# Kernel optimization log

Measured on AMD Instinct MI355X. Metric: run time of the kernel, lower is better.

## Reference

```python
import jax, jax.numpy as jnp
import numpy as np

N_SRC = 100000   # source nodes (columns of adj)
N_DST = 50000    # target nodes (rows of adj)
N_EDGES = 3200000
N_IN = 256
N_OUT = 128


def setup_inputs() -> dict:
    key = jax.random.key(0)
    k = jax.random.split(key, 7)
    stdv = 1.0 / np.sqrt(N_IN)
    x = jax.random.normal(k[0], (N_SRC, N_IN), dtype=jnp.float32)
    W = jax.random.uniform(k[1], (N_OUT, N_IN), minval=-stdv, maxval=stdv, dtype=jnp.float32)
    b = jax.random.uniform(k[2], (N_OUT,), minval=-stdv, maxval=stdv, dtype=jnp.float32)
    adj_rows = jax.random.randint(k[3], (N_EDGES,), 0, N_DST)
    adj_cols = jax.random.randint(k[4], (N_EDGES,), 0, N_SRC)
    # mean-aggregation-style normalized weights (generic positive values)
    adj_vals = jax.random.uniform(k[5], (N_EDGES,), dtype=jnp.float32)
    previous_index = jax.random.randint(k[6], (N_DST,), 0, N_SRC)
    return {"x": x, "W": W, "b": b, "adj_vals": adj_vals,
            "adj_rows": adj_rows, "adj_cols": adj_cols,
            "previous_index": previous_index}


def reference(x, W, b, adj_vals, adj_rows, adj_cols, previous_index):
    # linear projection: h = x @ W.T + b            -> [N_SRC, n_out]
    h = jnp.einsum('ni,oi->no', x, W) + b
    # spmm(adj, h) via COO gather + segment-sum      -> [N_DST, n_out]
    msgs = adj_vals[:, None] * h[adj_cols]          # [E, n_out]
    support = jax.ops.segment_sum(msgs, adj_rows, num_segments=previous_index.shape[0])
    # gather self features and concat                -> [N_DST, 2*n_out]
    return jnp.concatenate([h[previous_index], support], axis=1)
```

## Files before the change

### kernel.cpp

```cpp
#include <hip/hip_runtime.h>
#include <hip/hip_bf16.h>

#define N_IN      256
#define N_OUTC    128
#define RPS       64
#define RPS_SHIFT 6
#define NSB_MAX   1024
#define TILE      4096
#define EPT       16
#define SPILL_CAP 8192

typedef __attribute__((ext_vector_type(8))) short bf16x8;
typedef __attribute__((ext_vector_type(4))) float f32x4;
typedef unsigned short ushort_t;
typedef unsigned int uint_t;

__device__ inline unsigned short f2bf(float f) {
    unsigned u = __float_as_uint(f);
    unsigned r = u + 0x7fffu + ((u >> 16) & 1u);
    return (unsigned short)(r >> 16);
}
__device__ inline float bf_lo(uint_t g) { return __uint_as_float(g << 16); }
__device__ inline float bf_hi(uint_t g) { return __uint_as_float(g & 0xFFFF0000u); }

__global__ void cvtW_kernel(const float* __restrict__ W, ushort_t* __restrict__ wb, int n) {
    int i = blockIdx.x * blockDim.x + threadIdx.x;
    if (i < n) wb[i] = f2bf(W[i]);
}

__global__ __launch_bounds__(256) void fused_build_gemm_kernel(
        const int* __restrict__ rows, const int* __restrict__ cols,
        const float* __restrict__ vals, int E,
        int* __restrict__ sbCount, int2* __restrict__ sbList, int sbCap, int nsb,
        int* __restrict__ spillCnt, int4* __restrict__ spill, int nbBuild,
        const float* __restrict__ x, const ushort_t* __restrict__ wb,
        const float* __restrict__ b, ushort_t* __restrict__ h16) {
    __shared__ int cur[NSB_MAX];
    __shared__ int gbase[NSB_MAX];
    const int tid = threadIdx.x;

    if (blockIdx.x < (uint_t)nbBuild) {
        const int base = blockIdx.x * TILE;
        for (int i = tid; i < nsb; i += 256) cur[i] = 0;
        __syncthreads();

        int comb[EPT];
        #pragma unroll
        for (int k = 0; k < EPT; k++) {
            int e = base + tid + k * 256;
            comb[k] = -1;
            if (e < E) {
                int sb = rows[e] >> RPS_SHIFT;
                int rk = atomicAdd(&cur[sb], 1);
                comb[k] = (sb << 13) | rk;
            }
        }
        __syncthreads();

        for (int i = tid; i < nsb; i += 256)
            gbase[i] = cur[i] ? atomicAdd(&sbCount[i], cur[i]) : 0;
        __syncthreads();

        #pragma unroll
        for (int k = 0; k < EPT; k++) {
            if (comb[k] < 0) continue;
            int e  = base + tid + k * 256;
            int sb = ((uint_t)comb[k]) >> 13;
            int rk = comb[k] & 0x1FFF;
            int r = rows[e], c = cols[e];
            int ev = __float_as_int(vals[e]);
            int pos = gbase[sb] + rk;
            if (pos < sbCap) {
                sbList[(size_t)sb * sbCap + pos] = make_int2(c | ((r & (RPS - 1)) << 17), ev);
            } else {
                int sp = atomicAdd(spillCnt, 1);
                if (sp < SPILL_CAP)
                    spill[sp] = make_int4(r, c, ev, 0);
            }
        }
        return;
    }

    const int blk  = blockIdx.x - nbBuild;
    const int wave = tid >> 6;
    const int lane = tid & 63;
    const int quad = lane >> 4;
    const int l16  = lane & 15;
    const int m0   = blk * 16;
    const int colbase = wave * 32;

    f32x4 acc0 = {0.f, 0.f, 0.f, 0.f};
    f32x4 acc1 = {0.f, 0.f, 0.f, 0.f};

    const float* xrow = x + (size_t)(m0 + l16) * N_IN + quad * 8;
    const ushort_t* w0 = wb + (size_t)(colbase + l16) * N_IN + quad * 8;
    const ushort_t* w1 = w0 + 16 * N_IN;

    #pragma unroll
    for (int kb = 0; kb < N_IN; kb += 32) {
        float4 a0 = *(const float4*)(xrow + kb);
        float4 a1 = *(const float4*)(xrow + kb + 4);
        union { bf16x8 v; __hip_bfloat162 h2[4]; } u;
        u.h2[0] = __float22bfloat162_rn(make_float2(a0.x, a0.y));
        u.h2[1] = __float22bfloat162_rn(make_float2(a0.z, a0.w));
        u.h2[2] = __float22bfloat162_rn(make_float2(a1.x, a1.y));
        u.h2[3] = __float22bfloat162_rn(make_float2(a1.z, a1.w));
        bf16x8 bf0 = *(const bf16x8*)(w0 + kb);
        bf16x8 bf1 = *(const bf16x8*)(w1 + kb);
        acc0 = __builtin_amdgcn_mfma_f32_16x16x32_bf16(u.v, bf0, acc0, 0, 0, 0);
        acc1 = __builtin_amdgcn_mfma_f32_16x16x32_bf16(u.v, bf1, acc1, 0, 0, 0);
    }

    const int c0 = colbase + l16;
    const int c1 = c0 + 16;
    const float bv0 = b[c0];
    const float bv1 = b[c1];
    ushort_t* hp = h16 + (size_t)(m0 + quad * 4) * N_OUTC;
    #pragma unroll
    for (int r = 0; r < 4; r++) {
        hp[(size_t)r * N_OUTC + c0] = f2bf(acc0[r] + bv0);
        hp[(size_t)r * N_OUTC + c1] = f2bf(acc1[r] + bv1);
    }
}

__global__ __launch_bounds__(1024) void sbscan_kernel(const int* __restrict__ sbCount, int sbCap,
                                                      int* __restrict__ sbBase, int nsb) {
    __shared__ int a[NSB_MAX], bsh[NSB_MAX];
    int tid = threadIdx.x;
    int v = 0;
    if (tid < nsb) { v = sbCount[tid]; if (v > sbCap) v = sbCap; }
    a[tid] = v; __syncthreads();
    int* src = a; int* dst = bsh;
    for (int off = 1; off < 1024; off <<= 1) {
        dst[tid] = src[tid] + ((tid >= off) ? src[tid - off] : 0);
        __syncthreads();
        int* t = src; src = dst; dst = t;
    }
    if (tid < nsb) sbBase[tid] = tid ? src[tid - 1] : 0;
}

__global__ __launch_bounds__(256) void sort_kernel(const int* __restrict__ sbCount,
                                                   const int* __restrict__ sbBase,
                                                   const int2* __restrict__ sbList, int sbCap,
                                                   int2* __restrict__ csr,
                                                   int* __restrict__ rowStart, int* __restrict__ rowCnt,
                                                   int Ndst) {
    __shared__ int hist[RPS];
    __shared__ int scanA[RPS];
    __shared__ int curx[RPS];
    const int sb  = blockIdx.x;
    const int tid = threadIdx.x;
    int len = sbCount[sb]; if (len > sbCap) len = sbCap;
    const int base = sbBase[sb];
    const int2* lp = sbList + (size_t)sb * sbCap;

    if (tid < RPS) hist[tid] = 0;
    __syncthreads();

    int i = tid;
    for (; i + 768 < len; i += 1024) {
        int x0 = lp[i].x, x1 = lp[i + 256].x, x2 = lp[i + 512].x, x3 = lp[i + 768].x;
        atomicAdd(&hist[((uint_t)x0) >> 17], 1);
        atomicAdd(&hist[((uint_t)x1) >> 17], 1);
        atomicAdd(&hist[((uint_t)x2) >> 17], 1);
        atomicAdd(&hist[((uint_t)x3) >> 17], 1);
    }
    for (; i < len; i += 256) atomicAdd(&hist[((uint_t)lp[i].x) >> 17], 1);
    __syncthreads();

    if (tid < RPS) scanA[tid] = hist[tid];
    __syncthreads();
    for (int off = 1; off < RPS; off <<= 1) {
        int t = 0;
        if (tid < RPS) t = scanA[tid] + ((tid >= off) ? scanA[tid - off] : 0);
        __syncthreads();
        if (tid < RPS) scanA[tid] = t;
        __syncthreads();
    }
    if (tid < RPS) {
        int excl = tid ? scanA[tid - 1] : 0;
        curx[tid] = excl;
        int r = sb * RPS + tid;
        if (r < Ndst) { rowStart[r] = base + excl; rowCnt[r] = hist[tid]; }
    }
    __syncthreads();

    i = tid;
    for (; i + 768 < len; i += 1024) {
        int2 e0 = lp[i], e1 = lp[i + 256], e2 = lp[i + 512], e3 = lp[i + 768];
        int p0 = atomicAdd(&curx[((uint_t)e0.x) >> 17], 1);
        int p1 = atomicAdd(&curx[((uint_t)e1.x) >> 17], 1);
        int p2 = atomicAdd(&curx[((uint_t)e2.x) >> 17], 1);
        int p3 = atomicAdd(&curx[((uint_t)e3.x) >> 17], 1);
        csr[(size_t)base + p0] = make_int2(e0.x & 0x1FFFF, e0.y);
        csr[(size_t)base + p1] = make_int2(e1.x & 0x1FFFF, e1.y);
        csr[(size_t)base + p2] = make_int2(e2.x & 0x1FFFF, e2.y);
        csr[(size_t)base + p3] = make_int2(e3.x & 0x1FFFF, e3.y);
    }
    for (; i < len; i += 256) {
        int2 e = lp[i];
        int pos = atomicAdd(&curx[((uint_t)e.x) >> 17], 1);
        csr[(size_t)base + pos] = make_int2(e.x & 0x1FFFF, e.y);
    }
}

__global__ __launch_bounds__(256) void spmm_concat_kernel(const ushort_t* __restrict__ h16,
                                                          const int* __restrict__ rowStart,
                                                          const int* __restrict__ rowCnt,
                                                          const int2* __restrict__ csr,
                                                          const int* __restrict__ prev,
                                                          float* __restrict__ out, int Ndst) {
    int r = blockIdx.x * 4 + (threadIdx.x >> 6);
    if (r >= Ndst) return;
    const int lane = threadIdx.x & 63;
    const int cnt = rowCnt[r];
    const int2* bk = csr + rowStart[r];

    float2 acc = {0.f, 0.f};
    for (int bse = 0; bse < cnt; bse += 64) {
        int idx = bse + lane;
        int2 my = make_int2(0, 0);
        if (idx < cnt) my = bk[idx];
        int m = cnt - bse; if (m > 64) m = 64;
        int mg = (m + 7) & ~7;
        for (int j = 0; j < mg; j += 8) {
            int c0 = __shfl(my.x, j + 0), c1 = __shfl(my.x, j + 1);
            int c2 = __shfl(my.x, j + 2), c3 = __shfl(my.x, j + 3);
            int c4 = __shfl(my.x, j + 4), c5 = __shfl(my.x, j + 5);
            int c6 = __shfl(my.x, j + 6), c7 = __shfl(my.x, j + 7);
            uint_t g0 = *(const uint_t*)(h16 + (size_t)c0 * N_OUTC + 2 * lane);
            uint_t g1 = *(const uint_t*)(h16 + (size_t)c1 * N_OUTC + 2 * lane);
            uint_t g2 = *(const uint_t*)(h16 + (size_t)c2 * N_OUTC + 2 * lane);
            uint_t g3 = *(const uint_t*)(h16 + (size_t)c3 * N_OUTC + 2 * lane);
            uint_t g4 = *(const uint_t*)(h16 + (size_t)c4 * N_OUTC + 2 * lane);
            uint_t g5 = *(const uint_t*)(h16 + (size_t)c5 * N_OUTC + 2 * lane);
            uint_t g6 = *(const uint_t*)(h16 + (size_t)c6 * N_OUTC + 2 * lane);
            uint_t g7 = *(const uint_t*)(h16 + (size_t)c7 * N_OUTC + 2 * lane);
            float v0 = __int_as_float(__shfl(my.y, j + 0));
            float v1 = __int_as_float(__shfl(my.y, j + 1));
            float v2 = __int_as_float(__shfl(my.y, j + 2));
            float v3 = __int_as_float(__shfl(my.y, j + 3));
            float v4 = __int_as_float(__shfl(my.y, j + 4));
            float v5 = __int_as_float(__shfl(my.y, j + 5));
            float v6 = __int_as_float(__shfl(my.y, j + 6));
            float v7 = __int_as_float(__shfl(my.y, j + 7));
            acc.x += v0 * bf_lo(g0); acc.y += v0 * bf_hi(g0);
            acc.x += v1 * bf_lo(g1); acc.y += v1 * bf_hi(g1);
            acc.x += v2 * bf_lo(g2); acc.y += v2 * bf_hi(g2);
            acc.x += v3 * bf_lo(g3); acc.y += v3 * bf_hi(g3);
            acc.x += v4 * bf_lo(g4); acc.y += v4 * bf_hi(g4);
            acc.x += v5 * bf_lo(g5); acc.y += v5 * bf_hi(g5);
            acc.x += v6 * bf_lo(g6); acc.y += v6 * bf_hi(g6);
            acc.x += v7 * bf_lo(g7); acc.y += v7 * bf_hi(g7);
        }
    }

    int p = prev[r];
    uint_t g = *(const uint_t*)(h16 + (size_t)p * N_OUTC + 2 * lane);
    float2* o = (float2*)(out + (size_t)r * 256);
    o[lane]      = make_float2(bf_lo(g), bf_hi(g));
    o[64 + lane] = make_float2(acc.x, acc.y);
}

__global__ void spill_kernel(const ushort_t* __restrict__ h16, const int4* __restrict__ spill,
                             const int* __restrict__ spillCnt, float* __restrict__ out) {
    int n = *spillCnt; if (n > SPILL_CAP) n = SPILL_CAP;
    int total = n * 64;
    for (int t = blockIdx.x * blockDim.x + threadIdx.x; t < total; t += gridDim.x * blockDim.x) {
        int idx = t >> 6, lane = t & 63;
        int4 s = spill[idx];
        uint_t g = *(const uint_t*)(h16 + (size_t)s.y * N_OUTC + 2 * lane);
        float v = __int_as_float(s.z);
        atomicAdd(&out[(size_t)s.x * 256 + 128 + 2 * lane],     v * bf_lo(g));
        atomicAdd(&out[(size_t)s.x * 256 + 128 + 2 * lane + 1], v * bf_hi(g));
    }
}

__global__ __launch_bounds__(256) void gemm_only_kernel(const float* __restrict__ x,
                                                        const ushort_t* __restrict__ wb,
                                                        const float* __restrict__ b,
                                                        ushort_t* __restrict__ h16) {
    const int tid  = threadIdx.x;
    const int wave = tid >> 6;
    const int lane = tid & 63;
    const int quad = lane >> 4;
    const int l16  = lane & 15;
    const int m0   = blockIdx.x * 16;
    const int colbase = wave * 32;
    f32x4 acc0 = {0.f, 0.f, 0.f, 0.f};
    f32x4 acc1 = {0.f, 0.f, 0.f, 0.f};
    const float* xrow = x + (size_t)(m0 + l16) * N_IN + quad * 8;
    const ushort_t* w0 = wb + (size_t)(colbase + l16) * N_IN + quad * 8;
    const ushort_t* w1 = w0 + 16 * N_IN;
    #pragma unroll
    for (int kb = 0; kb < N_IN; kb += 32) {
        float4 a0 = *(const float4*)(xrow + kb);
        float4 a1 = *(const float4*)(xrow + kb + 4);
        union { bf16x8 v; __hip_bfloat162 h2[4]; } u;
        u.h2[0] = __float22bfloat162_rn(make_float2(a0.x, a0.y));
        u.h2[1] = __float22bfloat162_rn(make_float2(a0.z, a0.w));
        u.h2[2] = __float22bfloat162_rn(make_float2(a1.x, a1.y));
        u.h2[3] = __float22bfloat162_rn(make_float2(a1.z, a1.w));
        bf16x8 bf0 = *(const bf16x8*)(w0 + kb);
        bf16x8 bf1 = *(const bf16x8*)(w1 + kb);
        acc0 = __builtin_amdgcn_mfma_f32_16x16x32_bf16(u.v, bf0, acc0, 0, 0, 0);
        acc1 = __builtin_amdgcn_mfma_f32_16x16x32_bf16(u.v, bf1, acc1, 0, 0, 0);
    }
    const int c0 = colbase + l16;
    const int c1 = c0 + 16;
    const float bv0 = b[c0];
    const float bv1 = b[c1];
    ushort_t* hp = h16 + (size_t)(m0 + quad * 4) * N_OUTC;
    #pragma unroll
    for (int r = 0; r < 4; r++) {
        hp[(size_t)r * N_OUTC + c0] = f2bf(acc0[r] + bv0);
        hp[(size_t)r * N_OUTC + c1] = f2bf(acc1[r] + bv1);
    }
}

__global__ void concat_only_kernel(const ushort_t* __restrict__ h16, const int* __restrict__ prev,
                                   float* __restrict__ out, int Ndst) {
    int t = blockIdx.x * blockDim.x + threadIdx.x;
    int r = t >> 6, lane = t & 63;
    if (r >= Ndst) return;
    uint_t g = *(const uint_t*)(h16 + (size_t)prev[r] * N_OUTC + 2 * lane);
    ((float2*)out)[(size_t)r * 128 + lane] = make_float2(bf_lo(g), bf_hi(g));
}

__global__ void spmm_atomic_kernel(const ushort_t* __restrict__ h16, const int* __restrict__ rows,
                                   const int* __restrict__ cols, const float* __restrict__ vals,
                                   int E, float* __restrict__ out) {
    long long t = (long long)blockIdx.x * blockDim.x + threadIdx.x;
    int e = (int)(t >> 6), lane = (int)(t & 63);
    if (e >= E) return;
    uint_t g = *(const uint_t*)(h16 + (size_t)cols[e] * N_OUTC + 2 * lane);
    float v = vals[e];
    int r = rows[e];
    atomicAdd(&out[(size_t)r * 256 + 128 + 2 * lane],     v * bf_lo(g));
    atomicAdd(&out[(size_t)r * 256 + 128 + 2 * lane + 1], v * bf_hi(g));
}

extern "C" void kernel_launch(void* const* d_in, const int* in_sizes, int n_in,
                              void* d_out, int out_size, void* d_ws, size_t ws_size,
                              hipStream_t stream) {
    const float* x    = (const float*)d_in[0];
    const float* W    = (const float*)d_in[1];
    const float* b    = (const float*)d_in[2];
    const float* vals = (const float*)d_in[3];
    const int*   rows = (const int*)d_in[4];
    const int*   cols = (const int*)d_in[5];
    const int*   prev = (const int*)d_in[6];
    float* out = (float*)d_out;

    const int Nsrc = in_sizes[0] / N_IN;
    const int E    = in_sizes[3];
    const int Ndst = in_sizes[6];
    const int NSB  = (Ndst + RPS - 1) / RPS;
    const int sbCap = E / NSB + 516;
    const int nbBuild = (E + TILE - 1) / TILE;
    const int gemmBlocks = Nsrc / 16;

    char* ws = (char*)d_ws;
    size_t off = 0;
    ushort_t* h16 = (ushort_t*)(ws + off);
    off += (size_t)Nsrc * N_OUTC * sizeof(ushort_t);
    ushort_t* wb = (ushort_t*)(ws + off);
    off += (size_t)N_OUTC * N_IN * sizeof(ushort_t);
    off = (off + 255) & ~(size_t)255;
    int* sbCount  = (int*)(ws + off);
    int* spillCnt = sbCount + NSB;
    size_t memsetBytes = ((size_t)NSB + 1) * sizeof(int);
    off += memsetBytes;
    off = (off + 255) & ~(size_t)255;
    int* sbBase = (int*)(ws + off);
    off += (size_t)NSB * sizeof(int);
    off = (off + 255) & ~(size_t)255;
    int* rowStart = (int*)(ws + off);
    off += (size_t)Ndst * sizeof(int);
    int* rowCnt = (int*)(ws + off);
    off += (size_t)Ndst * sizeof(int);
    off = (off + 255) & ~(size_t)255;
    int4* spill = (int4*)(ws + off);
    off += (size_t)SPILL_CAP * sizeof(int4);
    off = (off + 255) & ~(size_t)255;
    int2* sbList = (int2*)(ws + off);
    off += (size_t)NSB * sbCap * sizeof(int2);
    off = (off + 255) & ~(size_t)255;
    int2* csr = (int2*)(ws + off);
    off += (size_t)E * sizeof(int2);

    cvtW_kernel<<<(N_OUTC * N_IN + 255) / 256, 256, 0, stream>>>(W, wb, N_OUTC * N_IN);

    if (off <= ws_size && NSB <= NSB_MAX) {
        hipMemsetAsync(sbCount, 0, memsetBytes, stream);
        fused_build_gemm_kernel<<<nbBuild + gemmBlocks, 256, 0, stream>>>(
            rows, cols, vals, E, sbCount, sbList, sbCap, NSB, spillCnt, spill, nbBuild,
            x, wb, b, h16);
        sbscan_kernel<<<1, 1024, 0, stream>>>(sbCount, sbCap, sbBase, NSB);
        sort_kernel<<<NSB, 256, 0, stream>>>(sbCount, sbBase, sbList, sbCap,
                                             csr, rowStart, rowCnt, Ndst);
        spmm_concat_kernel<<<(Ndst + 3) / 4, 256, 0, stream>>>(h16, rowStart, rowCnt, csr,
                                                               prev, out, Ndst);
        spill_kernel<<<64, 256, 0, stream>>>(h16, spill, spillCnt, out);
    } else {
        gemm_only_kernel<<<gemmBlocks, 256, 0, stream>>>(x, wb, b, h16);
        hipMemsetAsync(out, 0, (size_t)out_size * sizeof(float), stream);
        concat_only_kernel<<<((size_t)Ndst * 64 + 255) / 256, 256, 0, stream>>>(h16, prev, out, Ndst);
        spmm_atomic_kernel<<<((size_t)E * 64 + 255) / 256, 256, 0, stream>>>(h16, rows, cols, vals, E, out);
    }
}
```

Measured before the change: 476.6 us.

## Merge scan into sort kernel, fold spill into SpMM, enlarge build tiles

Removes the separate single-block scan kernel by having each 1024-thread sort block reduce the counts of the preceding superblocks itself. The spill kernel is also dropped: each SpMM row now scans the spill list and adds matching entries locally. The build phase switches to larger tiles with a two-pass count-then-scatter scheme, which cuts global atomics on sbCount. The cost is that every sort block re-reads up to 1024 counts, and every SpMM wave loops over the spill count. The larger tiles also mean fewer build blocks and less parallelism.

```diff
diff --git a/kernel.cpp b/kernel.cpp
--- a/kernel.cpp
+++ b/kernel.cpp
@@ -6,8 +6,7 @@
 #define RPS       64
 #define RPS_SHIFT 6
 #define NSB_MAX   1024
-#define TILE      4096
-#define EPT       16
+#define TILE      25000
 #define SPILL_CAP 8192
 
 typedef __attribute__((ext_vector_type(8))) short bf16x8;
@@ -41,41 +40,41 @@
 
     if (blockIdx.x < (uint_t)nbBuild) {
         const int base = blockIdx.x * TILE;
+        int e1 = base + TILE; if (e1 > E) e1 = E;
         for (int i = tid; i < nsb; i += 256) cur[i] = 0;
         __syncthreads();
 
-        int comb[EPT];
-        #pragma unroll
-        for (int k = 0; k < EPT; k++) {
-            int e = base + tid + k * 256;
-            comb[k] = -1;
-            if (e < E) {
-                int sb = rows[e] >> RPS_SHIFT;
-                int rk = atomicAdd(&cur[sb], 1);
-                comb[k] = (sb << 13) | rk;
-            }
-        }
-        __syncthreads();
-
-        for (int i = tid; i < nsb; i += 256)
-            gbase[i] = cur[i] ? atomicAdd(&sbCount[i], cur[i]) : 0;
-        __syncthreads();
-
-        #pragma unroll
-        for (int k = 0; k < EPT; k++) {
-            if (comb[k] < 0) continue;
-            int e  = base + tid + k * 256;
-            int sb = ((uint_t)comb[k]) >> 13;
-            int rk = comb[k] & 0x1FFF;
+        int e = base + tid;
+        for (; e + 768 < e1; e += 1024) {
+            int r0 = rows[e], r1 = rows[e + 256], r2 = rows[e + 512], r3 = rows[e + 768];
+            atomicAdd(&cur[r0 >> RPS_SHIFT], 1);
+            atomicAdd(&cur[r1 >> RPS_SHIFT], 1);
+            atomicAdd(&cur[r2 >> RPS_SHIFT], 1);
+            atomicAdd(&cur[r3 >> RPS_SHIFT], 1);
+        }
+        for (; e < e1; e += 256) atomicAdd(&cur[rows[e] >> RPS_SHIFT], 1);
+        __syncthreads();
+
+        for (int i = tid; i < nsb; i += 256) {
+            int c = cur[i];
+            gbase[i] = c ? atomicAdd(&sbCount[i], c) : 0;
+        }
+        __syncthreads();
+        for (int i = tid; i < nsb; i += 256) cur[i] = 0;
+        __syncthreads();
+
+        e = base + tid;
+        for (; e < e1; e += 256) {
             int r = rows[e], c = cols[e];
             int ev = __float_as_int(vals[e]);
+            int sb = r >> RPS_SHIFT;
+            int rk = atomicAdd(&cur[sb], 1);
             int pos = gbase[sb] + rk;
             if (pos < sbCap) {
                 sbList[(size_t)sb * sbCap + pos] = make_int2(c | ((r & (RPS - 1)) << 17), ev);
             } else {
                 int sp = atomicAdd(spillCnt, 1);
-                if (sp < SPILL_CAP)
-                    spill[sp] = make_int4(r, c, ev, 0);
+                if (sp < SPILL_CAP) spill[sp] = make_int4(r, c, ev, 0);
             }
         }
         return;
@@ -123,49 +122,43 @@
     }
 }
 
-__global__ __launch_bounds__(1024) void sbscan_kernel(const int* __restrict__ sbCount, int sbCap,
-                                                      int* __restrict__ sbBase, int nsb) {
-    __shared__ int a[NSB_MAX], bsh[NSB_MAX];
-    int tid = threadIdx.x;
-    int v = 0;
-    if (tid < nsb) { v = sbCount[tid]; if (v > sbCap) v = sbCap; }
-    a[tid] = v; __syncthreads();
-    int* src = a; int* dst = bsh;
-    for (int off = 1; off < 1024; off <<= 1) {
-        dst[tid] = src[tid] + ((tid >= off) ? src[tid - off] : 0);
-        __syncthreads();
-        int* t = src; src = dst; dst = t;
-    }
-    if (tid < nsb) sbBase[tid] = tid ? src[tid - 1] : 0;
-}
-
-__global__ __launch_bounds__(256) void sort_kernel(const int* __restrict__ sbCount,
-                                                   const int* __restrict__ sbBase,
-                                                   const int2* __restrict__ sbList, int sbCap,
-                                                   int2* __restrict__ csr,
-                                                   int* __restrict__ rowStart, int* __restrict__ rowCnt,
-                                                   int Ndst) {
+__global__ __launch_bounds__(1024) void sort_kernel(const int* __restrict__ sbCount,
+                                                    const int2* __restrict__ sbList, int sbCap,
+                                                    int2* __restrict__ csr,
+                                                    int* __restrict__ rowStart, int* __restrict__ rowCnt,
+                                                    int nsb, int Ndst) {
+    __shared__ int red[1024];
     __shared__ int hist[RPS];
     __shared__ int scanA[RPS];
     __shared__ int curx[RPS];
     const int sb  = blockIdx.x;
     const int tid = threadIdx.x;
+
+    int v = 0;
+    if (tid < sb) { v = sbCount[tid]; if (v > sbCap) v = sbCap; }
+    red[tid] = v; __syncthreads();
+    #pragma unroll
+    for (int off = 512; off > 0; off >>= 1) {
+        if (tid < off) red[tid] += red[tid + off];
+        __syncthreads();
+    }
+    const int base = red[0];
+
     int len = sbCount[sb]; if (len > sbCap) len = sbCap;
-    const int base = sbBase[sb];
     const int2* lp = sbList + (size_t)sb * sbCap;
 
     if (tid < RPS) hist[tid] = 0;
     __syncthreads();
 
     int i = tid;
-    for (; i + 768 < len; i += 1024) {
-        int x0 = lp[i].x, x1 = lp[i + 256].x, x2 = lp[i + 512].x, x3 = lp[i + 768].x;
+    for (; i + 3072 < len; i += 4096) {
+        int x0 = lp[i].x, x1 = lp[i + 1024].x, x2 = lp[i + 2048].x, x3 = lp[i + 3072].x;
         atomicAdd(&hist[((uint_t)x0) >> 17], 1);
         atomicAdd(&hist[((uint_t)x1) >> 17], 1);
         atomicAdd(&hist[((uint_t)x2) >> 17], 1);
         atomicAdd(&hist[((uint_t)x3) >> 17], 1);
     }
-    for (; i < len; i += 256) atomicAdd(&hist[((uint_t)lp[i].x) >> 17], 1);
+    for (; i < len; i += 1024) atomicAdd(&hist[((uint_t)lp[i].x) >> 17], 1);
     __syncthreads();
 
     if (tid < RPS) scanA[tid] = hist[tid];
@@ -186,8 +179,8 @@
     __syncthreads();
 
     i = tid;
-    for (; i + 768 < len; i += 1024) {
-        int2 e0 = lp[i], e1 = lp[i + 256], e2 = lp[i + 512], e3 = lp[i + 768];
+    for (; i + 3072 < len; i += 4096) {
+        int2 e0 = lp[i], e1 = lp[i + 1024], e2 = lp[i + 2048], e3 = lp[i + 3072];
         int p0 = atomicAdd(&curx[((uint_t)e0.x) >> 17], 1);
         int p1 = atomicAdd(&curx[((uint_t)e1.x) >> 17], 1);
         int p2 = atomicAdd(&curx[((uint_t)e2.x) >> 17], 1);
@@ -197,7 +190,7 @@
         csr[(size_t)base + p2] = make_int2(e2.x & 0x1FFFF, e2.y);
         csr[(size_t)base + p3] = make_int2(e3.x & 0x1FFFF, e3.y);
     }
-    for (; i < len; i += 256) {
+    for (; i < len; i += 1024) {
         int2 e = lp[i];
         int pos = atomicAdd(&curx[((uint_t)e.x) >> 17], 1);
         csr[(size_t)base + pos] = make_int2(e.x & 0x1FFFF, e.y);
@@ -209,6 +202,8 @@
                                                           const int* __restrict__ rowCnt,
                                                           const int2* __restrict__ csr,
                                                           const int* __restrict__ prev,
+                                                          const int* __restrict__ spillCnt,
+                                                          const int4* __restrict__ spill,
                                                           float* __restrict__ out, int Ndst) {
     int r = blockIdx.x * 4 + (threadIdx.x >> 6);
     if (r >= Ndst) return;
@@ -255,25 +250,21 @@
         }
     }
 
+    int nsp = *spillCnt; if (nsp > SPILL_CAP) nsp = SPILL_CAP;
+    for (int s = 0; s < nsp; s++) {
+        int4 sp = spill[s];
+        if (sp.x == r) {
+            uint_t g = *(const uint_t*)(h16 + (size_t)sp.y * N_OUTC + 2 * lane);
+            float v = __int_as_float(sp.z);
+            acc.x += v * bf_lo(g); acc.y += v * bf_hi(g);
+        }
+    }
+
     int p = prev[r];
     uint_t g = *(const uint_t*)(h16 + (size_t)p * N_OUTC + 2 * lane);
     float2* o = (float2*)(out + (size_t)r * 256);
     o[lane]      = make_float2(bf_lo(g), bf_hi(g));
     o[64 + lane] = make_float2(acc.x, acc.y);
-}
-
-__global__ void spill_kernel(const ushort_t* __restrict__ h16, const int4* __restrict__ spill,
-                             const int* __restrict__ spillCnt, float* __restrict__ out) {
-    int n = *spillCnt; if (n > SPILL_CAP) n = SPILL_CAP;
-    int total = n * 64;
-    for (int t = blockIdx.x * blockDim.x + threadIdx.x; t < total; t += gridDim.x * blockDim.x) {
-        int idx = t >> 6, lane = t & 63;
-        int4 s = spill[idx];
-        uint_t g = *(const uint_t*)(h16 + (size_t)s.y * N_OUTC + 2 * lane);
-        float v = __int_as_float(s.z);
-        atomicAdd(&out[(size_t)s.x * 256 + 128 + 2 * lane],     v * bf_lo(g));
-        atomicAdd(&out[(size_t)s.x * 256 + 128 + 2 * lane + 1], v * bf_hi(g));
-    }
 }
 
 __global__ __launch_bounds__(256) void gemm_only_kernel(const float* __restrict__ x,
@@ -372,9 +363,6 @@
     size_t memsetBytes = ((size_t)NSB + 1) * sizeof(int);
     off += memsetBytes;
     off = (off + 255) & ~(size_t)255;
-    int* sbBase = (int*)(ws + off);
-    off += (size_t)NSB * sizeof(int);
-    off = (off + 255) & ~(size_t)255;
     int* rowStart = (int*)(ws + off);
     off += (size_t)Ndst * sizeof(int);
     int* rowCnt = (int*)(ws + off);
@@ -396,12 +384,10 @@
         fused_build_gemm_kernel<<<nbBuild + gemmBlocks, 256, 0, stream>>>(
             rows, cols, vals, E, sbCount, sbList, sbCap, NSB, spillCnt, spill, nbBuild,
             x, wb, b, h16);
-        sbscan_kernel<<<1, 1024, 0, stream>>>(sbCount, sbCap, sbBase, NSB);
-        sort_kernel<<<NSB, 256, 0, stream>>>(sbCount, sbBase, sbList, sbCap,
-                                             csr, rowStart, rowCnt, Ndst);
+        sort_kernel<<<NSB, 1024, 0, stream>>>(sbCount, sbList, sbCap,
+                                              csr, rowStart, rowCnt, NSB, Ndst);
         spmm_concat_kernel<<<(Ndst + 3) / 4, 256, 0, stream>>>(h16, rowStart, rowCnt, csr,
-                                                               prev, out, Ndst);
-        spill_kernel<<<64, 256, 0, stream>>>(h16, spill, spillCnt, out);
+                                                               prev, spillCnt, spill, out, Ndst);
     } else {
         gemm_only_kernel<<<gemmBlocks, 256, 0, stream>>>(x, wb, b, h16);
         hipMemsetAsync(out, 0, (size_t)out_size * sizeof(float), stream);
```

Measured after the change: 468.2 us. Within noise of the previous version (-1.8%).
